# Optimization experiments

Hardware: AMD Instinct MI355X
Metric: run time of the kernel (lower is better)

The kernel has to match this reference:

```python
import jax, jax.numpy as jnp
import numpy as np

B, S, D, H = 4, 2048, 512, 4


def setup_inputs() -> dict:
    key = jax.random.key(0)
    ks = jax.random.split(key, 12)
    sd = 1.0 / np.sqrt(D)
    def lin(k, i, o):
        return jax.random.uniform(k, (i, o), jnp.float32, -sd, sd)
    return {
        "fencs": jax.random.normal(ks[0], (B, S, D), jnp.float32),
        # per-head Q/K/V projections, stacked over H heads: [H, D, D] (+ bias [H, D])
        "Wq": jnp.stack([lin(jax.random.fold_in(ks[1], h), D, D) for h in range(H)]),
        "bq": jax.random.uniform(ks[2], (H, D), jnp.float32, -sd, sd),
        "Wk": jnp.stack([lin(jax.random.fold_in(ks[3], h), D, D) for h in range(H)]),
        "bk": jax.random.uniform(ks[4], (H, D), jnp.float32, -sd, sd),
        "Wv": jnp.stack([lin(jax.random.fold_in(ks[5], h), D, D) for h in range(H)]),
        "bv": jax.random.uniform(ks[6], (H, D), jnp.float32, -sd, sd),
        # FFN: dims -> 4*dims -> dims, residual
        "W1": lin(ks[7], D, 4 * D),
        "b1": jax.random.uniform(ks[8], (4 * D,), jnp.float32, -sd, sd),
        "W2": lin(ks[9], 4 * D, D),
        "b2": jax.random.uniform(ks[10], (D,), jnp.float32, -sd, sd),
    }


def reference(fencs, Wq, bq, Wk, bk, Wv, bv, W1, b1, W2, b2):
    d = fencs.shape[-1]
    scale = 1.0 / jnp.sqrt(jnp.asarray(d, fencs.dtype))
    # batched per-head projections: [B,H,S,D]
    q = jnp.einsum("bsd,hde->bhse", fencs, Wq) + bq[None, :, None, :]
    k = jnp.einsum("bsd,hde->bhse", fencs, Wk) + bk[None, :, None, :]
    v = jnp.einsum("bsd,hde->bhse", fencs, Wv) + bv[None, :, None, :]
    scores = jnp.einsum("bhse,bhte->bhst", q, k) * scale  # [B,H,S,S]
    probs = jax.nn.softmax(scores, axis=-1)
    ctx = jnp.einsum("bhst,bhte->bhse", probs, v)  # [B,H,S,D]
    att = jnp.mean(ctx, axis=1)  # sum over heads / nheads -> [B,S,D]
    # FFN with residual around the FFN (residual input is the attention output)
    hid = jax.nn.relu(att @ W1 + b1)
    return att + (hid @ W2 + b2)
```

## Files before the change

### kernel.cpp

```cpp
#include <hip/hip_runtime.h>
#include <hip/hip_bf16.h>

typedef __attribute__((ext_vector_type(8))) short bf16x8;
typedef __attribute__((ext_vector_type(4))) float f32x4;

constexpr int Bc = 4, Sc = 2048, Dc = 512, Hc = 4;
constexpr float SCALE = 0.044194173824159216f;

__device__ __forceinline__ unsigned short f2bf(float f) {
  union { float f; unsigned u; } v; v.f = f;
  unsigned r = v.u + 0x7fffu + ((v.u >> 16) & 1u);
  return (unsigned short)(r >> 16);
}

#define GLD16(GP, LP) __builtin_amdgcn_global_load_lds( \
    (const __attribute__((address_space(1))) unsigned int*)(GP), \
    (__attribute__((address_space(3))) unsigned int*)(LP), 16, 0, 0)

__global__ __launch_bounds__(256) void k_cvt(const float* __restrict__ x,
                                             unsigned short* __restrict__ y, int n4,
                                             float scale) {
  int i = blockIdx.x * 256 + threadIdx.x;
  if (i < n4) {
    float4 v = ((const float4*)x)[i];
    ushort4 o;
    o.x = f2bf(v.x * scale); o.y = f2bf(v.y * scale);
    o.z = f2bf(v.z * scale); o.w = f2bf(v.w * scale);
    ((ushort4*)y)[i] = o;
  }
}

__global__ __launch_bounds__(256) void k_zero(float* __restrict__ p, int n4) {
  int i = blockIdx.x * 256 + threadIdx.x;
  if (i < n4) ((float4*)p)[i] = float4{0.f, 0.f, 0.f, 0.f};
}

__global__ __launch_bounds__(256) void k_fin(const float* __restrict__ x,
                                             unsigned short* __restrict__ y, int n4) {
  int i = blockIdx.x * 256 + threadIdx.x;
  if (i < n4) {
    float4 v = ((const float4*)x)[i];
    ushort4 o;
    o.x = f2bf(v.x); o.y = f2bf(v.y); o.z = f2bf(v.z); o.w = f2bf(v.w);
    ((ushort4*)y)[i] = o;
  }
}

__global__ __launch_bounds__(256) void k_wt(const float* __restrict__ W,
                                            unsigned short* __restrict__ WT,
                                            int K_, int N_, float scale) {
  const int z = blockIdx.z;
  W  += (size_t)z * K_ * N_;
  WT += (size_t)z * K_ * N_;
  __shared__ float t[32][33];
  const int k0 = blockIdx.x * 32, n0 = blockIdx.y * 32;
  const int tx = threadIdx.x & 31, ty = threadIdx.x >> 5;
#pragma unroll
  for (int i = 0; i < 32; i += 8) t[ty + i][tx] = W[(size_t)(k0 + ty + i) * N_ + n0 + tx];
  __syncthreads();
#pragma unroll
  for (int i = 0; i < 32; i += 8)
    WT[(size_t)(n0 + ty + i) * K_ + k0 + tx] = f2bf(t[tx][ty + i] * scale);
}

__global__ __launch_bounds__(256) void k_vecmat(const float* __restrict__ bqv,
                                                const float* __restrict__ Wk,
                                                float* __restrict__ cvec) {
  const int g = blockIdx.x * 256 + threadIdx.x;
  const int h = g >> 9, d = g & 511;
  const float* wr = Wk + ((size_t)h * 512 + d) * 512;
  const float* bb = bqv + h * 512;
  float s = 0.f;
  for (int e = 0; e < 512; e += 4) {
    const float4 w = *(const float4*)(wr + e);
    const float4 q = *(const float4*)(bb + e);
    s += w.x * q.x + w.y * q.y + w.z * q.z + w.w * q.w;
  }
  cvec[g] = s * SCALE;
}

enum { EPI_MT = 0, EPI_QK = 1, EPI_V = 2, EPI_EXP = 3, EPI_PV = 4, EPI_RELU = 5, EPI_OUT = 6 };

template <int EPI>
__global__ __launch_bounds__(256)
void k_gemm(const unsigned short* __restrict__ A, size_t sA,
            const unsigned short* __restrict__ BTg, size_t sB, int bzsh,
            const float* __restrict__ bias,
            void* __restrict__ outv, float* __restrict__ extra, int K)
{
  const int tid = threadIdx.x;
  const int w = tid >> 6, l = tid & 63;
  const int l15 = l & 15, lg = l >> 4;
  const int mb = blockIdx.x * 128, nb = blockIdx.y * 128;
  const int z = blockIdx.z;
  const int h = z;
  const unsigned short* Ae = A + (size_t)z * sA;
  const unsigned short* Be = BTg + (size_t)(z >> bzsh) * sB;

  __shared__ __align__(16) unsigned short As0[128 * 64], As1[128 * 64];
  __shared__ __align__(16) unsigned short Bs0[128 * 64], Bs1[128 * 64];

  f32x4 acc[4][4] = {};
  const int wm = w >> 1, wn = w & 1;
  const int mw = wm * 64, nw = wn * 64;
  const int nkt = K >> 6;

  auto stage = [&](int kb, unsigned short* Ad, unsigned short* Bd) {
#pragma unroll
    for (int i = 0; i < 4; ++i) {
      const int chunk = (w * 4 + i) * 64 + l;
      const int row = chunk >> 3;
      const int sb = ((chunk & 7) * 16) ^ ((row & 7) << 4);
      GLD16(Ae + (size_t)(mb + row) * K + kb + (sb >> 1), (char*)Ad + (w * 4 + i) * 1024);
      GLD16(Be + (size_t)(nb + row) * K + kb + (sb >> 1), (char*)Bd + (w * 4 + i) * 1024);
    }
  };
  auto compute = [&](const unsigned short* Asb, const unsigned short* Bsb) {
#pragma unroll
    for (int ks = 0; ks < 2; ++ks) {
      bf16x8 af[4], bfr[4];
#pragma unroll
      for (int m = 0; m < 4; ++m) {
        const int row = mw + m * 16 + l15;
        const int off = (ks * 64 + lg * 16) ^ ((row & 7) << 4);
        af[m] = *(const bf16x8*)((const char*)Asb + row * 128 + off);
      }
#pragma unroll
      for (int n = 0; n < 4; ++n) {
        const int row = nw + n * 16 + l15;
        const int off = (ks * 64 + lg * 16) ^ ((row & 7) << 4);
        bfr[n] = *(const bf16x8*)((const char*)Bsb + row * 128 + off);
      }
#pragma unroll
      for (int m = 0; m < 4; ++m)
#pragma unroll
        for (int n = 0; n < 4; ++n)
          acc[m][n] = __builtin_amdgcn_mfma_f32_16x16x32_bf16(af[m], bfr[n], acc[m][n], 0, 0, 0);
    }
  };

  stage(0, As0, Bs0);
  __syncthreads();
  for (int kt = 0; kt < nkt; kt += 2) {
    if (kt + 1 < nkt) stage((kt + 1) << 6, As1, Bs1);
    compute(As0, Bs0);
    __syncthreads();
    if (kt + 2 < nkt) stage((kt + 2) << 6, As0, Bs0);
    compute(As1, Bs1);
    __syncthreads();
  }

  if constexpr (EPI == EPI_MT) {
    unsigned short* op = (unsigned short*)outv;
#pragma unroll
    for (int m = 0; m < 4; ++m)
#pragma unroll
      for (int n = 0; n < 4; ++n) {
        const int col = nb + nw + n * 16 + l15;
#pragma unroll
        for (int r = 0; r < 4; ++r) {
          const int row = mb + mw + m * 16 + lg * 4 + r;
          op[((size_t)z * 512 + row) * 512 + col] = f2bf(acc[m][n][r]);
        }
      }
  } else if constexpr (EPI == EPI_QK || EPI == EPI_V) {
    unsigned short* op = (unsigned short*)outv;
#pragma unroll
    for (int m = 0; m < 4; ++m) {
#pragma unroll
      for (int n = 0; n < 4; ++n) {
        const int col = nb + nw + n * 16 + l15;
        const float bv = bias[h * Dc + col];
#pragma unroll
        for (int r = 0; r < 4; ++r) {
          const int row = mb + mw + m * 16 + lg * 4 + r;
          const float v = acc[m][n][r] + bv;
          const int bb = row >> 11, s = row & 2047;
          if constexpr (EPI == EPI_QK)
            op[(((size_t)bb * Hc + h) * Sc + s) * Dc + col] = f2bf(v);
          else
            op[(((size_t)bb * Hc + h) * Dc + col) * Sc + s] = f2bf(v);
        }
      }
    }
  } else if constexpr (EPI == EPI_EXP) {
    unsigned short* P = (unsigned short*)outv;
#pragma unroll
    for (int m = 0; m < 4; ++m) {
#pragma unroll
      for (int r = 0; r < 4; ++r) {
        const int row = mb + mw + m * 16 + lg * 4 + r;
        float ps = 0.f;
#pragma unroll
        for (int n = 0; n < 4; ++n) {
          const int col = nb + nw + n * 16 + l15;
          const float p = __expf(acc[m][n][r]);
          ps += p;
          P[((size_t)h * Sc + row) * Sc + col] = f2bf(p);
        }
#pragma unroll
        for (int d = 1; d < 16; d <<= 1) ps += __shfl_xor(ps, d);
        if (l15 == 0) atomicAdd(&extra[h * Sc + row], ps);
      }
    }
  } else if constexpr (EPI == EPI_PV) {
    float* of = (float*)outv + (size_t)(h >> 2) * 1048576;
#pragma unroll
    for (int m = 0; m < 4; ++m) {
#pragma unroll
      for (int r = 0; r < 4; ++r) {
        const int row = mb + mw + m * 16 + lg * 4 + r;
        const float il = 0.25f / extra[h * Sc + row];
#pragma unroll
        for (int n = 0; n < 4; ++n) {
          const int col = nb + nw + n * 16 + l15;
          atomicAdd(&of[(size_t)row * Dc + col], acc[m][n][r] * il);
        }
      }
    }
  } else if constexpr (EPI == EPI_RELU) {
#pragma unroll
    for (int m = 0; m < 4; ++m) {
#pragma unroll
      for (int n = 0; n < 4; ++n) {
        const int col = nb + nw + n * 16 + l15;
        const float bv = bias[col];
#pragma unroll
        for (int r = 0; r < 4; ++r) {
          const int row = mb + mw + m * 16 + lg * 4 + r;
          ((unsigned short*)outv)[(size_t)row * 2048 + col] = f2bf(fmaxf(acc[m][n][r] + bv, 0.f));
        }
      }
    }
  } else {
    float* of = (float*)outv;
#pragma unroll
    for (int m = 0; m < 4; ++m) {
#pragma unroll
      for (int n = 0; n < 4; ++n) {
        const int col = nb + nw + n * 16 + l15;
        const float bv = bias[col];
#pragma unroll
        for (int r = 0; r < 4; ++r) {
          const int row = mb + mw + m * 16 + lg * 4 + r;
          of[(size_t)row * Dc + col] = acc[m][n][r] + bv + extra[(size_t)row * Dc + col];
        }
      }
    }
  }
}

extern "C" void kernel_launch(void* const* d_in, const int* in_sizes, int n_in,
                              void* d_out, int out_size, void* d_ws, size_t ws_size,
                              hipStream_t stream)
{
  const float* fencs = (const float*)d_in[0];
  const float* Wq  = (const float*)d_in[1];
  const float* bq  = (const float*)d_in[2];
  const float* Wk  = (const float*)d_in[3];
  const float* bk  = (const float*)d_in[4];
  const float* Wv  = (const float*)d_in[5];
  const float* bvv = (const float*)d_in[6];
  const float* W1  = (const float*)d_in[7];
  const float* b1  = (const float*)d_in[8];
  const float* W2  = (const float*)d_in[9];
  const float* b2  = (const float*)d_in[10];
  float* out = (float*)d_out;
  (void)bk;

  if (ws_size < 134291456u) return;
  unsigned short* MTb = (unsigned short*)d_ws;
  unsigned short* WvT = MTb + (size_t)1048576;
  unsigned short* W1T = WvT + (size_t)1048576;
  unsigned short* W2T = W1T + (size_t)1048576;
  unsigned short* Xbf = W2T + (size_t)1048576;
  unsigned short* Qp  = Xbf + (size_t)4194304;
  unsigned short* VTp = Qp  + (size_t)8388608;
  unsigned short* P2  = VTp + (size_t)8388608;
  float* attf = (float*)(P2 + (size_t)33554432);
  float* lbuf = attf + (size_t)4194304;
  float* cvec = lbuf + (size_t)16384;
  unsigned short* Wqs  = W1T;
  unsigned short* Wkb  = W2T;
  unsigned short* attb = Qp;
  unsigned short* hid  = P2;

  k_cvt<<<4096, 256, 0, stream>>>(fencs, Xbf, 1048576, 1.0f);
  k_cvt<<<1024, 256, 0, stream>>>(Wq, Wqs, 262144, SCALE);
  k_cvt<<<1024, 256, 0, stream>>>(Wk, Wkb, 262144, 1.0f);
  k_vecmat<<<8, 256, 0, stream>>>(bq, Wk, cvec);
  k_gemm<EPI_MT><<<dim3(4, 4, 4), 256, 0, stream>>>(
      Wkb, 262144, Wqs, 262144, 0, nullptr, MTb, nullptr, 512);
  k_wt<<<dim3(16, 16, 4), 256, 0, stream>>>(Wv, WvT, 512, 512, 1.0f);
  k_zero<<<4096, 256, 0, stream>>>(attf, 1048576);

  for (int p = 0; p < 2; ++p) {
    const unsigned short* Xp = Xbf + (size_t)p * 2097152;
    k_gemm<EPI_QK><<<dim3(32, 4, 4), 256, 0, stream>>>(
        Xp, 0, MTb, 262144, 0, cvec, Qp, nullptr, 512);
    k_gemm<EPI_V><<<dim3(32, 4, 4), 256, 0, stream>>>(
        Xp, 0, WvT, 262144, 0, bvv, VTp, nullptr, 512);
    k_zero<<<16, 256, 0, stream>>>(lbuf, 4096);
    k_gemm<EPI_EXP><<<dim3(16, 16, 8), 256, 0, stream>>>(
        Qp, 1048576, Xp, 1048576, 2, nullptr, P2, lbuf, 512);
    k_gemm<EPI_PV><<<dim3(16, 4, 8), 256, 0, stream>>>(
        P2, 4194304, VTp, 1048576, 0, nullptr,
        attf + (size_t)p * 2097152, lbuf, 2048);
  }

  k_wt<<<dim3(16, 64, 1), 256, 0, stream>>>(W1, W1T, 512, 2048, 1.0f);
  k_wt<<<dim3(64, 16, 1), 256, 0, stream>>>(W2, W2T, 2048, 512, 1.0f);

  k_fin<<<4096, 256, 0, stream>>>(attf, attb, 1048576);

  k_gemm<EPI_RELU><<<dim3(64, 16, 1), 256, 0, stream>>>(
      attb, 0, W1T, 0, 0, b1, hid, nullptr, 512);
  k_gemm<EPI_OUT><<<dim3(64, 4, 1), 256, 0, stream>>>(
      hid, 0, W2T, 0, 0, b2, out, attf, 2048);
}
```

Baseline: 393.9 us.

## Add 256x256-tile 8-wave GEMM kernel for score-exp and FFN1 stages

Adds a new GEMM kernel, k_g8, that uses 512 threads, 256x256 output tiles, double-buffered LDS filled through global_load_lds, and interleaved B-tile staging with priority-raised MFMA blocks. The QK^T-exp stage and the first FFN GEMM now use it in place of the 128x128 k_gemm. The aim is more data reuse per loaded tile and better overlap of loads with MFMA work. The cost is higher register and LDS pressure (128KB LDS per block) and fewer blocks in each grid.

```diff
diff --git a/kernel.cpp b/kernel.cpp
--- a/kernel.cpp
+++ b/kernel.cpp
@@ -183,17 +183,143 @@
         }
       }
     }
-  } else if constexpr (EPI == EPI_EXP) {
-    unsigned short* P = (unsigned short*)outv;
+  } else if constexpr (EPI == EPI_PV) {
+    float* of = (float*)outv + (size_t)(h >> 2) * 1048576;
 #pragma unroll
     for (int m = 0; m < 4; ++m) {
 #pragma unroll
       for (int r = 0; r < 4; ++r) {
         const int row = mb + mw + m * 16 + lg * 4 + r;
-        float ps = 0.f;
+        const float il = 0.25f / extra[h * Sc + row];
 #pragma unroll
         for (int n = 0; n < 4; ++n) {
           const int col = nb + nw + n * 16 + l15;
+          atomicAdd(&of[(size_t)row * Dc + col], acc[m][n][r] * il);
+        }
+      }
+    }
+  } else {
+    float* of = (float*)outv;
+#pragma unroll
+    for (int m = 0; m < 4; ++m) {
+#pragma unroll
+      for (int n = 0; n < 4; ++n) {
+        const int col = nb + nw + n * 16 + l15;
+        const float bv = bias[col];
+#pragma unroll
+        for (int r = 0; r < 4; ++r) {
+          const int row = mb + mw + m * 16 + lg * 4 + r;
+          of[(size_t)row * Dc + col] = acc[m][n][r] + bv + extra[(size_t)row * Dc + col];
+        }
+      }
+    }
+  }
+}
+
+template <int EPI>
+__global__ __launch_bounds__(512, 2)
+void k_g8(const unsigned short* __restrict__ A, size_t sA,
+          const unsigned short* __restrict__ BTg, size_t sB, int bzsh,
+          const float* __restrict__ bias,
+          void* __restrict__ outv, float* __restrict__ extra, int K)
+{
+  const int tid = threadIdx.x;
+  const int w = tid >> 6, l = tid & 63;
+  const int l15 = l & 15, lg = l >> 4;
+  const int wm = w >> 2, wn = w & 3;
+  const int mb = blockIdx.x * 256, nb = blockIdx.y * 256;
+  const int z = blockIdx.z, h = z;
+  const unsigned short* Abase = A + (size_t)z * sA + (size_t)mb * K;
+  const unsigned short* Bbase = BTg + (size_t)(z >> bzsh) * sB + (size_t)nb * K;
+
+  __shared__ __align__(16) unsigned short As0[256 * 64], As1[256 * 64];
+  __shared__ __align__(16) unsigned short Bs0[256 * 64], Bs1[256 * 64];
+
+  f32x4 acc[8][4] = {};
+  const int nkt = K >> 6;
+
+  auto stg = [&](const unsigned short* gbase, int kb, unsigned short* dst, int half) {
+#pragma unroll
+    for (int s2 = 0; s2 < 2; ++s2) {
+      const int s = half * 2 + s2;
+      const int c = s * 512 + w * 64 + l;
+      const int row = c >> 3;
+      const int sb = ((c & 7) * 16) ^ ((row & 7) << 4);
+      GLD16(gbase + (size_t)row * K + kb + (sb >> 1), (char*)dst + s * 8192 + w * 1024);
+    }
+  };
+
+  stg(Abase, 0, As0, 0); stg(Abase, 0, As0, 1);
+  stg(Bbase, 0, Bs0, 0); stg(Bbase, 0, Bs0, 1);
+  __builtin_amdgcn_sched_barrier(0);
+
+  for (int t = 0; t < nkt; ++t) {
+    unsigned short* Asb = (t & 1) ? As1 : As0;
+    unsigned short* Bsb = (t & 1) ? Bs1 : Bs0;
+    unsigned short* Asn = (t & 1) ? As0 : As1;
+    unsigned short* Bsn = (t & 1) ? Bs0 : Bs1;
+    const int kbn = (t + 1 < nkt) ? (t + 1) << 6 : 0;
+
+    stg(Abase, kbn, Asn, 0);
+    stg(Abase, kbn, Asn, 1);
+    asm volatile("s_waitcnt vmcnt(4)" ::: "memory");
+    __builtin_amdgcn_sched_barrier(0);
+    __builtin_amdgcn_s_barrier();
+    __builtin_amdgcn_sched_barrier(0);
+
+    bf16x8 bfr[4][2];
+#pragma unroll
+    for (int n = 0; n < 4; ++n) {
+      const int row = wn * 64 + n * 16 + l15;
+#pragma unroll
+      for (int k = 0; k < 2; ++k) {
+        const int off = (k * 64 + lg * 16) ^ ((row & 7) << 4);
+        bfr[n][k] = *(const bf16x8*)((const char*)Bsb + row * 128 + off);
+      }
+    }
+#pragma unroll
+    for (int q = 0; q < 4; ++q) {
+      bf16x8 af[2][2];
+#pragma unroll
+      for (int mm = 0; mm < 2; ++mm) {
+        const int row = wm * 128 + (q * 2 + mm) * 16 + l15;
+#pragma unroll
+        for (int k = 0; k < 2; ++k) {
+          const int off = (k * 64 + lg * 16) ^ ((row & 7) << 4);
+          af[mm][k] = *(const bf16x8*)((const char*)Asb + row * 128 + off);
+        }
+      }
+      if (q == 0) stg(Bbase, kbn, Bsn, 0);
+      if (q == 1) stg(Bbase, kbn, Bsn, 1);
+      __builtin_amdgcn_s_barrier();
+      asm volatile("s_waitcnt lgkmcnt(0)" ::: "memory");
+      __builtin_amdgcn_sched_barrier(0);
+      __builtin_amdgcn_s_setprio(1);
+#pragma unroll
+      for (int mm = 0; mm < 2; ++mm)
+#pragma unroll
+        for (int n = 0; n < 4; ++n)
+#pragma unroll
+          for (int k = 0; k < 2; ++k)
+            acc[q * 2 + mm][n] = __builtin_amdgcn_mfma_f32_16x16x32_bf16(
+                af[mm][k], bfr[n][k], acc[q * 2 + mm][n], 0, 0, 0);
+      __builtin_amdgcn_s_setprio(0);
+      __builtin_amdgcn_sched_barrier(0);
+      __builtin_amdgcn_s_barrier();
+    }
+  }
+
+  if constexpr (EPI == EPI_EXP) {
+    unsigned short* P = (unsigned short*)outv;
+#pragma unroll
+    for (int m = 0; m < 8; ++m) {
+#pragma unroll
+      for (int r = 0; r < 4; ++r) {
+        const int row = mb + wm * 128 + m * 16 + lg * 4 + r;
+        float ps = 0.f;
+#pragma unroll
+        for (int n = 0; n < 4; ++n) {
+          const int col = nb + wn * 64 + n * 16 + l15;
           const float p = __expf(acc[m][n][r]);
           ps += p;
           P[((size_t)h * Sc + row) * Sc + col] = f2bf(p);
@@ -203,50 +329,19 @@
         if (l15 == 0) atomicAdd(&extra[h * Sc + row], ps);
       }
     }
-  } else if constexpr (EPI == EPI_PV) {
-    float* of = (float*)outv + (size_t)(h >> 2) * 1048576;
-#pragma unroll
-    for (int m = 0; m < 4; ++m) {
-#pragma unroll
-      for (int r = 0; r < 4; ++r) {
-        const int row = mb + mw + m * 16 + lg * 4 + r;
-        const float il = 0.25f / extra[h * Sc + row];
-#pragma unroll
-        for (int n = 0; n < 4; ++n) {
-          const int col = nb + nw + n * 16 + l15;
-          atomicAdd(&of[(size_t)row * Dc + col], acc[m][n][r] * il);
-        }
-      }
-    }
-  } else if constexpr (EPI == EPI_RELU) {
-#pragma unroll
-    for (int m = 0; m < 4; ++m) {
+  } else {
+#pragma unroll
+    for (int m = 0; m < 8; ++m)
 #pragma unroll
       for (int n = 0; n < 4; ++n) {
-        const int col = nb + nw + n * 16 + l15;
+        const int col = nb + wn * 64 + n * 16 + l15;
         const float bv = bias[col];
 #pragma unroll
         for (int r = 0; r < 4; ++r) {
-          const int row = mb + mw + m * 16 + lg * 4 + r;
+          const int row = mb + wm * 128 + m * 16 + lg * 4 + r;
           ((unsigned short*)outv)[(size_t)row * 2048 + col] = f2bf(fmaxf(acc[m][n][r] + bv, 0.f));
         }
       }
-    }
-  } else {
-    float* of = (float*)outv;
-#pragma unroll
-    for (int m = 0; m < 4; ++m) {
-#pragma unroll
-      for (int n = 0; n < 4; ++n) {
-        const int col = nb + nw + n * 16 + l15;
-        const float bv = bias[col];
-#pragma unroll
-        for (int r = 0; r < 4; ++r) {
-          const int row = mb + mw + m * 16 + lg * 4 + r;
-          of[(size_t)row * Dc + col] = acc[m][n][r] + bv + extra[(size_t)row * Dc + col];
-        }
-      }
-    }
   }
 }
 
@@ -301,7 +396,7 @@
     k_gemm<EPI_V><<<dim3(32, 4, 4), 256, 0, stream>>>(
         Xp, 0, WvT, 262144, 0, bvv, VTp, nullptr, 512);
     k_zero<<<16, 256, 0, stream>>>(lbuf, 4096);
-    k_gemm<EPI_EXP><<<dim3(16, 16, 8), 256, 0, stream>>>(
+    k_g8<EPI_EXP><<<dim3(8, 8, 8), 512, 0, stream>>>(
         Qp, 1048576, Xp, 1048576, 2, nullptr, P2, lbuf, 512);
     k_gemm<EPI_PV><<<dim3(16, 4, 8), 256, 0, stream>>>(
         P2, 4194304, VTp, 1048576, 0, nullptr,
@@ -313,7 +408,7 @@
 
   k_fin<<<4096, 256, 0, stream>>>(attf, attb, 1048576);
 
-  k_gemm<EPI_RELU><<<dim3(64, 16, 1), 256, 0, stream>>>(
+  k_g8<EPI_RELU><<<dim3(32, 8, 1), 512, 0, stream>>>(
       attb, 0, W1T, 0, 0, b1, hid, nullptr, 512);
   k_gemm<EPI_OUT><<<dim3(64, 4, 1), 256, 0, stream>>>(
       hid, 0, W2T, 0, 0, b2, out, attf, 2048);
```

New measurement: 405.7 us. +3.0%, slower.

## Merge Q/V projection GEMMs into one launch and split-K the final FFN GEMM

Applied to the files above, without the earlier changes.

The separate Q and V projection GEMMs become a single launch with z=8, where the first four z-slices write Q and the last four write transposed V. This relies on MTb and WvT sitting next to each other in the workspace, and on VTp sitting right after Qp. The final output GEMM now splits K=2048 into two halves across blockIdx.z and accumulates into a zeroed output with atomicAdd, doubling the block count from 256 to 512 to fill more CUs. The cost is an extra zeroing pass and atomic traffic, and the floating-point summation order becomes nondeterministic.

```diff
diff --git a/kernel.cpp b/kernel.cpp
--- a/kernel.cpp
+++ b/kernel.cpp
@@ -79,13 +79,13 @@
   cvec[g] = s * SCALE;
 }
 
-enum { EPI_MT = 0, EPI_QK = 1, EPI_V = 2, EPI_EXP = 3, EPI_PV = 4, EPI_RELU = 5, EPI_OUT = 6 };
+enum { EPI_MT = 0, EPI_QKV = 1, EPI_EXP = 2, EPI_PV = 3, EPI_RELU = 4, EPI_OUT2 = 5 };
 
 template <int EPI>
 __global__ __launch_bounds__(256)
 void k_gemm(const unsigned short* __restrict__ A, size_t sA,
             const unsigned short* __restrict__ BTg, size_t sB, int bzsh,
-            const float* __restrict__ bias,
+            const float* __restrict__ bias, const float* __restrict__ bias2,
             void* __restrict__ outv, float* __restrict__ extra, int K)
 {
   const int tid = threadIdx.x;
@@ -93,9 +93,14 @@
   const int l15 = l & 15, lg = l >> 4;
   const int mb = blockIdx.x * 128, nb = blockIdx.y * 128;
   const int z = blockIdx.z;
-  const int h = z;
-  const unsigned short* Ae = A + (size_t)z * sA;
-  const unsigned short* Be = BTg + (size_t)(z >> bzsh) * sB;
+  const int h = (EPI == EPI_QKV) ? (z & 3) : z;
+  const unsigned short* Ae = A + (size_t)((EPI == EPI_OUT2) ? 0 : z) * sA;
+  const unsigned short* Be;
+  if constexpr (EPI == EPI_QKV) Be = BTg + (size_t)z * 262144;
+  else if constexpr (EPI == EPI_OUT2) Be = BTg;
+  else Be = BTg + (size_t)(z >> bzsh) * sB;
+  const int kbase = (EPI == EPI_OUT2) ? z * 1024 : 0;
+  const int nkt = (EPI == EPI_OUT2) ? 16 : (K >> 6);
 
   __shared__ __align__(16) unsigned short As0[128 * 64], As1[128 * 64];
   __shared__ __align__(16) unsigned short Bs0[128 * 64], Bs1[128 * 64];
@@ -103,7 +108,6 @@
   f32x4 acc[4][4] = {};
   const int wm = w >> 1, wn = w & 1;
   const int mw = wm * 64, nw = wn * 64;
-  const int nkt = K >> 6;
 
   auto stage = [&](int kb, unsigned short* Ad, unsigned short* Bd) {
 #pragma unroll
@@ -111,8 +115,8 @@
       const int chunk = (w * 4 + i) * 64 + l;
       const int row = chunk >> 3;
       const int sb = ((chunk & 7) * 16) ^ ((row & 7) << 4);
-      GLD16(Ae + (size_t)(mb + row) * K + kb + (sb >> 1), (char*)Ad + (w * 4 + i) * 1024);
-      GLD16(Be + (size_t)(nb + row) * K + kb + (sb >> 1), (char*)Bd + (w * 4 + i) * 1024);
+      GLD16(Ae + (size_t)(mb + row) * K + kbase + kb + (sb >> 1), (char*)Ad + (w * 4 + i) * 1024);
+      GLD16(Be + (size_t)(nb + row) * K + kbase + kb + (sb >> 1), (char*)Bd + (w * 4 + i) * 1024);
     }
   };
   auto compute = [&](const unsigned short* Asb, const unsigned short* Bsb) {
@@ -163,23 +167,24 @@
           op[((size_t)z * 512 + row) * 512 + col] = f2bf(acc[m][n][r]);
         }
       }
-  } else if constexpr (EPI == EPI_QK || EPI == EPI_V) {
+  } else if constexpr (EPI == EPI_QKV) {
     unsigned short* op = (unsigned short*)outv;
+    const bool isq = (z < 4);
 #pragma unroll
     for (int m = 0; m < 4; ++m) {
 #pragma unroll
       for (int n = 0; n < 4; ++n) {
         const int col = nb + nw + n * 16 + l15;
-        const float bv = bias[h * Dc + col];
+        const float bv = isq ? bias[h * Dc + col] : bias2[h * Dc + col];
 #pragma unroll
         for (int r = 0; r < 4; ++r) {
           const int row = mb + mw + m * 16 + lg * 4 + r;
           const float v = acc[m][n][r] + bv;
           const int bb = row >> 11, s = row & 2047;
-          if constexpr (EPI == EPI_QK)
+          if (isq)
             op[(((size_t)bb * Hc + h) * Sc + s) * Dc + col] = f2bf(v);
           else
-            op[(((size_t)bb * Hc + h) * Dc + col) * Sc + s] = f2bf(v);
+            op[8388608 + (((size_t)bb * Hc + h) * Dc + col) * Sc + s] = f2bf(v);
         }
       }
     }
@@ -243,7 +248,9 @@
 #pragma unroll
         for (int r = 0; r < 4; ++r) {
           const int row = mb + mw + m * 16 + lg * 4 + r;
-          of[(size_t)row * Dc + col] = acc[m][n][r] + bv + extra[(size_t)row * Dc + col];
+          float v = acc[m][n][r];
+          if (z == 0) v += bv + extra[(size_t)row * Dc + col];
+          atomicAdd(&of[(size_t)row * Dc + col], v);
         }
       }
     }
@@ -290,21 +297,19 @@
   k_cvt<<<1024, 256, 0, stream>>>(Wk, Wkb, 262144, 1.0f);
   k_vecmat<<<8, 256, 0, stream>>>(bq, Wk, cvec);
   k_gemm<EPI_MT><<<dim3(4, 4, 4), 256, 0, stream>>>(
-      Wkb, 262144, Wqs, 262144, 0, nullptr, MTb, nullptr, 512);
+      Wkb, 262144, Wqs, 262144, 0, nullptr, nullptr, MTb, nullptr, 512);
   k_wt<<<dim3(16, 16, 4), 256, 0, stream>>>(Wv, WvT, 512, 512, 1.0f);
   k_zero<<<4096, 256, 0, stream>>>(attf, 1048576);
 
   for (int p = 0; p < 2; ++p) {
     const unsigned short* Xp = Xbf + (size_t)p * 2097152;
-    k_gemm<EPI_QK><<<dim3(32, 4, 4), 256, 0, stream>>>(
-        Xp, 0, MTb, 262144, 0, cvec, Qp, nullptr, 512);
-    k_gemm<EPI_V><<<dim3(32, 4, 4), 256, 0, stream>>>(
-        Xp, 0, WvT, 262144, 0, bvv, VTp, nullptr, 512);
+    k_gemm<EPI_QKV><<<dim3(32, 4, 8), 256, 0, stream>>>(
+        Xp, 0, MTb, 0, 0, cvec, bvv, Qp, nullptr, 512);
     k_zero<<<16, 256, 0, stream>>>(lbuf, 4096);
     k_gemm<EPI_EXP><<<dim3(16, 16, 8), 256, 0, stream>>>(
-        Qp, 1048576, Xp, 1048576, 2, nullptr, P2, lbuf, 512);
+        Qp, 1048576, Xp, 1048576, 2, nullptr, nullptr, P2, lbuf, 512);
     k_gemm<EPI_PV><<<dim3(16, 4, 8), 256, 0, stream>>>(
-        P2, 4194304, VTp, 1048576, 0, nullptr,
+        P2, 4194304, VTp, 1048576, 0, nullptr, nullptr,
         attf + (size_t)p * 2097152, lbuf, 2048);
   }
 
@@ -314,7 +319,8 @@
   k_fin<<<4096, 256, 0, stream>>>(attf, attb, 1048576);
 
   k_gemm<EPI_RELU><<<dim3(64, 16, 1), 256, 0, stream>>>(
-      attb, 0, W1T, 0, 0, b1, hid, nullptr, 512);
-  k_gemm<EPI_OUT><<<dim3(64, 4, 1), 256, 0, stream>>>(
-      hid, 0, W2T, 0, 0, b2, out, attf, 2048);
-}
+      attb, 0, W1T, 0, 0, b1, nullptr, hid, nullptr, 512);
+  k_zero<<<4096, 256, 0, stream>>>(out, 1048576);
+  k_gemm<EPI_OUT2><<<dim3(64, 4, 2), 256, 0, stream>>>(
+      hid, 0, W2T, 0, 0, b2, nullptr, out, attf, 2048);
+}
```

New measurement: 443.7 us. 12.6% more time.
